# Performance work log

Hardware: AMD Instinct MI355X
Metric: run time of the kernel (lower is better)

## Reference

```python
import jax, jax.numpy as jnp
import numpy as np

H_FEATS = 256
N_NODES = 100000
N_EDGES = 1000000
EDGE_FEAT_DIM = 7
OUT_DIM = 4


def setup_inputs() -> dict:
    key = jax.random.key(0)
    ks = jax.random.split(key, 8)
    h = jax.random.normal(ks[0], (N_NODES, H_FEATS), dtype=jnp.float32)
    edge_feat = jax.random.normal(ks[1], (N_EDGES, EDGE_FEAT_DIM), dtype=jnp.float32)
    src = jax.random.randint(ks[2], (N_EDGES,), 0, N_NODES, dtype=jnp.int64)
    dst = jax.random.randint(ks[3], (N_EDGES,), 0, N_NODES, dtype=jnp.int64)
    in_dim = 2 * H_FEATS + EDGE_FEAT_DIM  # 519
    # Kaiming-ish init scale for the linear layers
    W1_w = jax.random.normal(ks[4], (in_dim, H_FEATS), dtype=jnp.float32) / np.sqrt(in_dim)
    W1_b = jax.random.normal(ks[5], (H_FEATS,), dtype=jnp.float32) * 0.01
    W2_w = jax.random.normal(ks[6], (H_FEATS, OUT_DIM), dtype=jnp.float32) / np.sqrt(H_FEATS)
    W2_b = jax.random.normal(ks[7], (OUT_DIM,), dtype=jnp.float32) * 0.01
    return {"h": h, "edge_feat": edge_feat, "src": src, "dst": dst,
            "W1_w": W1_w, "W1_b": W1_b, "W2_w": W2_w, "W2_b": W2_b}


def reference(h, edge_feat, src, dst, W1_w, W1_b, W2_w, W2_b):
    # Gather src/dst node embeddings per edge, concat with edge features: [E, 2*h_feats+7]
    x = jnp.concatenate([edge_feat, h[src], h[dst]], axis=1)
    # 2-layer MLP per edge: Linear -> ReLU -> Linear
    hid = jax.nn.relu(x @ W1_w + W1_b)          # [E, h_feats]
    rep = hid @ W2_w + W2_b                     # [E, 4]
    return rep
```

## Files before the change

### kernel.cpp

```cpp
#include <hip/hip_runtime.h>
#include <stdint.h>

#define NODES 100000
#define EDGES 1000000
#define HF 256
#define TILES2 (EDGES / 32)


typedef short short8 __attribute__((ext_vector_type(8)));
typedef float f32x4 __attribute__((ext_vector_type(4)));
typedef float f32x2 __attribute__((ext_vector_type(2)));
typedef int i32x4 __attribute__((ext_vector_type(4)));

__device__ __forceinline__ unsigned short f2b(float f) {
  union { float f; uint32_t u; } v; v.f = f;
  return (unsigned short)((v.u + 0x7FFFu + ((v.u >> 16) & 1u)) >> 16);
}
__device__ __forceinline__ float asf(uint32_t u) {
  union { uint32_t u; float f; } v; v.u = u;
  return v.f;
}
__device__ __forceinline__ uint32_t cvtpk(float lo, float hi) {
  uint32_t pk;
  asm("v_cvt_pk_bf16_f32 %0, %1, %2" : "=v"(pk) : "v"(lo), "v"(hi));
  return pk;
}

__global__ __launch_bounds__(256) void pack_w1(const float* __restrict__ W1,
                                               unsigned short* __restrict__ Bp) {
  int idx = blockIdx.x * 256 + threadIdx.x;
  int lane = idx & 63;
  int nbg  = (idx >> 6) & 31;
  int kb   = idx >> 11;
  int n    = nbg * 16 + (lane & 15);
  int k0   = kb * 32 + (lane >> 4) * 8;
  int rbase = (n < 256) ? 7 : 263;
  int col   = n & 255;
  short8 o;
#pragma unroll
  for (int j = 0; j < 8; ++j)
    o[j] = (short)f2b(W1[(size_t)(rbase + k0 + j) * HF + col]);
  *reinterpret_cast<short8*>(Bp + (size_t)idx * 8) = o;
}

__global__ __launch_bounds__(256, 1) void gemm_R(const float* __restrict__ h,
                                                 const unsigned short* __restrict__ Bp,
                                                 const float* __restrict__ b1,
                                                 unsigned short* __restrict__ R) {
  __shared__ unsigned short A[64][264];
  const int m0 = blockIdx.x * 64;
  const int t  = threadIdx.x;
  {
    const int r = t >> 2, q = t & 3;
    const int grow = m0 + r;
    const bool valid = grow < NODES;
    const float* hp = h + (size_t)grow * HF + q * 64;
#pragma unroll
    for (int cc = 0; cc < 8; ++cc) {
      float4 a, b;
      if (valid) {
        a = *reinterpret_cast<const float4*>(hp + cc * 8);
        b = *reinterpret_cast<const float4*>(hp + cc * 8 + 4);
      } else {
        a = make_float4(0.f, 0.f, 0.f, 0.f);
        b = a;
      }
      uint32_t o32[4];
      o32[0] = cvtpk(a.x, a.y);
      o32[1] = cvtpk(a.z, a.w);
      o32[2] = cvtpk(b.x, b.y);
      o32[3] = cvtpk(b.z, b.w);
      *reinterpret_cast<uint4*>(&A[r][q * 64 + cc * 8]) =
          make_uint4(o32[0], o32[1], o32[2], o32[3]);
    }
  }
  __syncthreads();

  const int wave = t >> 6, lane = t & 63;
  const int l15 = lane & 15, lhi = lane >> 4;
  const int nbg0 = wave * 8;
  f32x4 acc[4][8] = {};
#pragma unroll
  for (int kb = 0; kb < 8; ++kb) {
    short8 bfrag[8];
#pragma unroll
    for (int nb = 0; nb < 8; ++nb)
      bfrag[nb] = *reinterpret_cast<const short8*>(
          Bp + (((size_t)(kb * 32 + nbg0 + nb) * 64 + lane) * 8));
    short8 afrag[4];
#pragma unroll
    for (int mb = 0; mb < 4; ++mb)
      afrag[mb] = *reinterpret_cast<const short8*>(&A[mb * 16 + l15][kb * 32 + lhi * 8]);
#pragma unroll
    for (int mb = 0; mb < 4; ++mb)
#pragma unroll
      for (int nb = 0; nb < 8; ++nb)
        acc[mb][nb] = __builtin_amdgcn_mfma_f32_16x16x32_bf16(
            afrag[mb], bfrag[nb], acc[mb][nb], 0, 0, 0);
  }
  const int c0 = wave * 128 + l15;
  float b1v[8] = {};
  if (wave < 2) {
#pragma unroll
    for (int nb = 0; nb < 8; ++nb) b1v[nb] = b1[c0 + nb * 16];
  }
#pragma unroll
  for (int mb = 0; mb < 4; ++mb) {
#pragma unroll
    for (int i = 0; i < 4; ++i) {
      const int row = m0 + mb * 16 + lhi * 4 + i;
      if (row < NODES) {
        unsigned short* rp = R + (size_t)row * 512 + c0;
#pragma unroll
        for (int nb = 0; nb < 8; ++nb) rp[nb * 16] = f2b(acc[mb][nb][i] + b1v[nb]);
      }
    }
  }
}

__global__ __launch_bounds__(256) void edge_mlp(
    const unsigned short* __restrict__ R, const float* __restrict__ ef,
    const int* __restrict__ src, const int* __restrict__ dst,
    const float* __restrict__ W1, const float* __restrict__ W2,
    const float* __restrict__ b2, float* __restrict__ out) {
  __shared__ float w1a[7 * 256];
  for (int i = threadIdx.x; i < 7 * 64; i += 256)
    reinterpret_cast<float4*>(w1a)[i] = reinterpret_cast<const float4*>(W1)[i];
  __syncthreads();

  const int lane = threadIdx.x & 63;
  const int l15 = lane & 15, lhi = lane >> 4;
  const int esub = lane >> 2;
  const int sub  = lane & 3;
  const int bperm_idx = ((((lane & 15) << 2) | (lane >> 4)) << 2);

  short8 bfrag[8];
#pragma unroll
  for (int kb = 0; kb < 8; ++kb) {
    short8 b = {0, 0, 0, 0, 0, 0, 0, 0};
    if (l15 < 4) {
#pragma unroll
      for (int j = 0; j < 8; ++j)
        b[j] = (short)f2b(W2[(size_t)(kb * 32 + lhi * 8 + j) * 4 + l15]);
    }
    bfrag[kb] = b;
  }
  const float b2l = (l15 < 4) ? b2[l15] : 0.f;

  const int wid = (blockIdx.x * blockDim.x + threadIdx.x) >> 6;
  const int nw  = (gridDim.x * blockDim.x) >> 6;

#define TILE_KB(PV, QV, EFV, ACC)                                              \
  {                                                                            \
    const uint32_t* pu = reinterpret_cast<const uint32_t*>(&PV);               \
    const uint32_t* qu = reinterpret_cast<const uint32_t*>(&QV);               \
    f32x2 hd[4];                                                               \
    _Pragma("unroll") for (int w = 0; w < 4; ++w) {                            \
      f32x2 p2 = {asf(pu[w] << 16), asf(pu[w] & 0xffff0000u)};                 \
      f32x2 q2 = {asf(qu[w] << 16), asf(qu[w] & 0xffff0000u)};                 \
      hd[w] = p2 + q2;                                                         \
    }                                                                          \
    _Pragma("unroll") for (int j = 0; j < 7; ++j) {                            \
      f32x2 e2 = {EFV[j], EFV[j]};                                             \
      hd[0] = wv[j][0] * e2 + hd[0];                                           \
      hd[1] = wv[j][1] * e2 + hd[1];                                           \
      hd[2] = wv[j][2] * e2 + hd[2];                                           \
      hd[3] = wv[j][3] * e2 + hd[3];                                           \
    }                                                                          \
    union { i32x4 i; short8 s8; } afm;                                         \
    _Pragma("unroll") for (int w = 0; w < 4; ++w) {                            \
      const float lo = fmaxf(hd[w][0], 0.f);                                   \
      const float hi = fmaxf(hd[w][1], 0.f);                                   \
      afm.i[w] = __builtin_amdgcn_ds_bpermute(bperm_idx, (int)cvtpk(lo, hi));  \
    }                                                                          \
    ACC = __builtin_amdgcn_mfma_f32_16x16x32_bf16(afm.s8, bfrag[kb], ACC, 0, 0, 0); \
  }

  for (int t = wid; t < TILES2; t += nw) {
    const int e0 = t * 32;
    const int eiA = e0 + esub;
    const int eiB = eiA + 16;
    const int sA = src[eiA], dA = dst[eiA];
    const int sB = src[eiB], dB = dst[eiB];
    float efA[7], efB[7];
#pragma unroll
    for (int j = 0; j < 7; ++j) {
      efA[j] = ef[(size_t)eiA * 7 + j];
      efB[j] = ef[(size_t)eiB * 7 + j];
    }
    const unsigned short* PpA = R + (size_t)sA * 512 + sub * 8;
    const unsigned short* QpA = R + (size_t)dA * 512 + 256 + sub * 8;
    const unsigned short* PpB = R + (size_t)sB * 512 + sub * 8;
    const unsigned short* QpB = R + (size_t)dB * 512 + 256 + sub * 8;

    short8 pA[8], qA[8], pB[8], qB[8];
#pragma unroll
    for (int kb = 0; kb < 2; ++kb) {
      pA[kb] = *reinterpret_cast<const short8*>(PpA + kb * 32);
      qA[kb] = *reinterpret_cast<const short8*>(QpA + kb * 32);
      pB[kb] = *reinterpret_cast<const short8*>(PpB + kb * 32);
      qB[kb] = *reinterpret_cast<const short8*>(QpB + kb * 32);
    }

    f32x4 accA = {}, accB = {};
#pragma unroll
    for (int kb = 0; kb < 8; ++kb) {
      if (kb < 6) {
        pA[kb + 2] = *reinterpret_cast<const short8*>(PpA + (kb + 2) * 32);
        qA[kb + 2] = *reinterpret_cast<const short8*>(QpA + (kb + 2) * 32);
        pB[kb + 2] = *reinterpret_cast<const short8*>(PpB + (kb + 2) * 32);
        qB[kb + 2] = *reinterpret_cast<const short8*>(QpB + (kb + 2) * 32);
      }
      f32x2 wv[7][4];
      const float* ws = w1a + kb * 32 + sub * 8;
#pragma unroll
      for (int j = 0; j < 7; ++j) {
        const float4 wa = *reinterpret_cast<const float4*>(ws + j * 256);
        const float4 wb = *reinterpret_cast<const float4*>(ws + j * 256 + 4);
        wv[j][0] = {wa.x, wa.y};
        wv[j][1] = {wa.z, wa.w};
        wv[j][2] = {wb.x, wb.y};
        wv[j][3] = {wb.z, wb.w};
      }
      TILE_KB(pA[kb], qA[kb], efA, accA);
      TILE_KB(pB[kb], qB[kb], efB, accB);
    }
    if (l15 < 4) {
#pragma unroll
      for (int i = 0; i < 4; ++i) {
        out[(size_t)(e0 + lhi * 4 + i) * 4 + l15] = accA[i] + b2l;
        out[(size_t)(e0 + 16 + lhi * 4 + i) * 4 + l15] = accB[i] + b2l;
      }
    }
  }
#undef TILE_KB
}

extern "C" void kernel_launch(void* const* d_in, const int* in_sizes, int n_in,
                              void* d_out, int out_size, void* d_ws, size_t ws_size,
                              hipStream_t stream) {
  const float* h  = (const float*)d_in[0];
  const float* ef = (const float*)d_in[1];
  const int* src  = (const int*)d_in[2];
  const int* dst  = (const int*)d_in[3];
  const float* W1 = (const float*)d_in[4];
  const float* b1 = (const float*)d_in[5];
  const float* W2 = (const float*)d_in[6];
  const float* b2 = (const float*)d_in[7];
  float* out = (float*)d_out;

  const size_t bp_bytes = (size_t)8 * 32 * 64 * 8 * 2;
  unsigned short* Bp = (unsigned short*)d_ws;
  unsigned short* R  = (unsigned short*)((char*)d_ws + bp_bytes);

  pack_w1<<<64, 256, 0, stream>>>(W1, Bp);
  gemm_R<<<(NODES + 63) / 64, 256, 0, stream>>>(h, Bp, b1, R);
  edge_mlp<<<2048, 256, 0, stream>>>(R, ef, src, dst, W1, W2, b2, out);
}
```

Baseline: 236.6 us.

## Counting-sort edges by source node and drop bpermute in the edge MLP

Each call now counting-sorts the edges by source node: a histogram, a two-level scan and an atomic scatter build 32-byte records holding src, dst, the original edge id and the edge features packed to bf16. The edge MLP reads these records, so consecutive edges share source rows of R and get better cache reuse, and it writes outputs back to the original edge positions. The lane-to-edge mapping changes so the MFMA A fragment is built directly in registers, removing the ds_bpermute. In exchange it adds several extra kernels, atomics, a 32 MB record buffer, scattered output stores, and rounds edge features to bf16.

```diff
diff --git a/kernel.cpp b/kernel.cpp
--- a/kernel.cpp
+++ b/kernel.cpp
@@ -5,6 +5,7 @@
 #define EDGES 1000000
 #define HF 256
 #define TILES2 (EDGES / 32)
+#define NBINS (98 * 1024)
 
 
 typedef short short8 __attribute__((ext_vector_type(8)));
@@ -19,6 +20,9 @@
 __device__ __forceinline__ float asf(uint32_t u) {
   union { uint32_t u; float f; } v; v.u = u;
   return v.f;
+}
+__device__ __forceinline__ float b2f(unsigned short s) {
+  return asf(((uint32_t)s) << 16);
 }
 __device__ __forceinline__ uint32_t cvtpk(float lo, float hi) {
   uint32_t pk;
@@ -118,11 +122,85 @@
   }
 }
 
+__global__ __launch_bounds__(256) void hist_k(const int* __restrict__ src,
+                                              int* __restrict__ bins) {
+  int e = blockIdx.x * 256 + threadIdx.x;
+  if (e < EDGES) atomicAdd(&bins[src[e]], 1);
+}
+
+__global__ __launch_bounds__(256) void scan_blocks(int* __restrict__ bins,
+                                                   int* __restrict__ part) {
+  __shared__ int sdata[256];
+  const int t = threadIdx.x;
+  const int base = blockIdx.x * 1024 + t * 4;
+  int4 v = *reinterpret_cast<int4*>(bins + base);
+  const int s = v.x + v.y + v.z + v.w;
+  sdata[t] = s;
+  __syncthreads();
+#pragma unroll
+  for (int off = 1; off < 256; off <<= 1) {
+    int x = (t >= off) ? sdata[t - off] : 0;
+    __syncthreads();
+    sdata[t] += x;
+    __syncthreads();
+  }
+  const int excl = sdata[t] - s;
+  int4 o;
+  o.x = excl; o.y = excl + v.x; o.z = o.y + v.y; o.w = o.z + v.z;
+  *reinterpret_cast<int4*>(bins + base) = o;
+  if (t == 255) part[blockIdx.x] = sdata[255];
+}
+
+__global__ __launch_bounds__(128) void scan_partials(int* __restrict__ part, int nb) {
+  __shared__ int sdata[128];
+  const int t = threadIdx.x;
+  const int v = (t < nb) ? part[t] : 0;
+  sdata[t] = v;
+  __syncthreads();
+#pragma unroll
+  for (int off = 1; off < 128; off <<= 1) {
+    int x = (t >= off) ? sdata[t - off] : 0;
+    __syncthreads();
+    sdata[t] += x;
+    __syncthreads();
+  }
+  if (t < nb) part[t] = sdata[t] - v;
+}
+
+__global__ __launch_bounds__(256) void add_offsets(int* __restrict__ bins,
+                                                   const int* __restrict__ part) {
+  const int add = part[blockIdx.x];
+  const int base = blockIdx.x * 1024 + threadIdx.x * 4;
+  int4 v = *reinterpret_cast<int4*>(bins + base);
+  v.x += add; v.y += add; v.z += add; v.w += add;
+  *reinterpret_cast<int4*>(bins + base) = v;
+}
+
+__global__ __launch_bounds__(256) void scatter_k(const int* __restrict__ src,
+                                                 const int* __restrict__ dst,
+                                                 const float* __restrict__ ef,
+                                                 int* __restrict__ bins,
+                                                 char* __restrict__ rec) {
+  int e = blockIdx.x * 256 + threadIdx.x;
+  if (e >= EDGES) return;
+  const int s = src[e];
+  const int r = atomicAdd(&bins[s], 1);
+  int4 meta;
+  meta.x = s; meta.y = dst[e]; meta.z = e; meta.w = 0;
+  short8 efp = {0, 0, 0, 0, 0, 0, 0, 0};
+#pragma unroll
+  for (int j = 0; j < 7; ++j) efp[j] = (short)f2b(ef[(size_t)e * 7 + j]);
+  *reinterpret_cast<int4*>(rec + (size_t)r * 32) = meta;
+  *reinterpret_cast<short8*>(rec + (size_t)r * 32 + 16) = efp;
+}
+
+template <bool SORTED>
 __global__ __launch_bounds__(256) void edge_mlp(
-    const unsigned short* __restrict__ R, const float* __restrict__ ef,
-    const int* __restrict__ src, const int* __restrict__ dst,
-    const float* __restrict__ W1, const float* __restrict__ W2,
-    const float* __restrict__ b2, float* __restrict__ out) {
+    const unsigned short* __restrict__ R, const char* __restrict__ rec,
+    const float* __restrict__ ef, const int* __restrict__ src,
+    const int* __restrict__ dst, const float* __restrict__ W1,
+    const float* __restrict__ W2, const float* __restrict__ b2,
+    float* __restrict__ out) {
   __shared__ float w1a[7 * 256];
   for (int i = threadIdx.x; i < 7 * 64; i += 256)
     reinterpret_cast<float4*>(w1a)[i] = reinterpret_cast<const float4*>(W1)[i];
@@ -130,9 +208,6 @@
 
   const int lane = threadIdx.x & 63;
   const int l15 = lane & 15, lhi = lane >> 4;
-  const int esub = lane >> 2;
-  const int sub  = lane & 3;
-  const int bperm_idx = ((((lane & 15) << 2) | (lane >> 4)) << 2);
 
   short8 bfrag[8];
 #pragma unroll
@@ -171,27 +246,41 @@
     _Pragma("unroll") for (int w = 0; w < 4; ++w) {                            \
       const float lo = fmaxf(hd[w][0], 0.f);                                   \
       const float hi = fmaxf(hd[w][1], 0.f);                                   \
-      afm.i[w] = __builtin_amdgcn_ds_bpermute(bperm_idx, (int)cvtpk(lo, hi));  \
+      afm.i[w] = (int)cvtpk(lo, hi);                                           \
     }                                                                          \
     ACC = __builtin_amdgcn_mfma_f32_16x16x32_bf16(afm.s8, bfrag[kb], ACC, 0, 0, 0); \
   }
 
   for (int t = wid; t < TILES2; t += nw) {
     const int e0 = t * 32;
-    const int eiA = e0 + esub;
+    const int eiA = e0 + l15;
     const int eiB = eiA + 16;
-    const int sA = src[eiA], dA = dst[eiA];
-    const int sB = src[eiB], dB = dst[eiB];
+    int sA, dA, sB, dB;
     float efA[7], efB[7];
-#pragma unroll
-    for (int j = 0; j < 7; ++j) {
-      efA[j] = ef[(size_t)eiA * 7 + j];
-      efB[j] = ef[(size_t)eiB * 7 + j];
-    }
-    const unsigned short* PpA = R + (size_t)sA * 512 + sub * 8;
-    const unsigned short* QpA = R + (size_t)dA * 512 + 256 + sub * 8;
-    const unsigned short* PpB = R + (size_t)sB * 512 + sub * 8;
-    const unsigned short* QpB = R + (size_t)dB * 512 + 256 + sub * 8;
+    if constexpr (SORTED) {
+      const int4 mA = *reinterpret_cast<const int4*>(rec + (size_t)eiA * 32);
+      const int4 mB = *reinterpret_cast<const int4*>(rec + (size_t)eiB * 32);
+      const short8 eA8 = *reinterpret_cast<const short8*>(rec + (size_t)eiA * 32 + 16);
+      const short8 eB8 = *reinterpret_cast<const short8*>(rec + (size_t)eiB * 32 + 16);
+      sA = mA.x; dA = mA.y; sB = mB.x; dB = mB.y;
+#pragma unroll
+      for (int j = 0; j < 7; ++j) {
+        efA[j] = b2f((unsigned short)eA8[j]);
+        efB[j] = b2f((unsigned short)eB8[j]);
+      }
+    } else {
+      sA = src[eiA]; dA = dst[eiA];
+      sB = src[eiB]; dB = dst[eiB];
+#pragma unroll
+      for (int j = 0; j < 7; ++j) {
+        efA[j] = ef[(size_t)eiA * 7 + j];
+        efB[j] = ef[(size_t)eiB * 7 + j];
+      }
+    }
+    const unsigned short* PpA = R + (size_t)sA * 512 + lhi * 8;
+    const unsigned short* QpA = R + (size_t)dA * 512 + 256 + lhi * 8;
+    const unsigned short* PpB = R + (size_t)sB * 512 + lhi * 8;
+    const unsigned short* QpB = R + (size_t)dB * 512 + 256 + lhi * 8;
 
     short8 pA[8], qA[8], pB[8], qB[8];
 #pragma unroll
@@ -212,7 +301,7 @@
         qB[kb + 2] = *reinterpret_cast<const short8*>(QpB + (kb + 2) * 32);
       }
       f32x2 wv[7][4];
-      const float* ws = w1a + kb * 32 + sub * 8;
+      const float* ws = w1a + kb * 32 + lhi * 8;
 #pragma unroll
       for (int j = 0; j < 7; ++j) {
         const float4 wa = *reinterpret_cast<const float4*>(ws + j * 256);
@@ -228,8 +317,17 @@
     if (l15 < 4) {
 #pragma unroll
       for (int i = 0; i < 4; ++i) {
-        out[(size_t)(e0 + lhi * 4 + i) * 4 + l15] = accA[i] + b2l;
-        out[(size_t)(e0 + 16 + lhi * 4 + i) * 4 + l15] = accB[i] + b2l;
+        const int rA = e0 + lhi * 4 + i;
+        const int rB = rA + 16;
+        if constexpr (SORTED) {
+          const int oA = *reinterpret_cast<const int*>(rec + (size_t)rA * 32 + 8);
+          const int oB = *reinterpret_cast<const int*>(rec + (size_t)rB * 32 + 8);
+          out[(size_t)oA * 4 + l15] = accA[i] + b2l;
+          out[(size_t)oB * 4 + l15] = accB[i] + b2l;
+        } else {
+          out[(size_t)rA * 4 + l15] = accA[i] + b2l;
+          out[(size_t)rB * 4 + l15] = accB[i] + b2l;
+        }
       }
     }
   }
@@ -249,11 +347,32 @@
   const float* b2 = (const float*)d_in[7];
   float* out = (float*)d_out;
 
-  const size_t bp_bytes = (size_t)8 * 32 * 64 * 8 * 2;
+  const size_t bp_bytes  = (size_t)8 * 32 * 64 * 8 * 2;
+  const size_t r_bytes   = (size_t)NODES * 512 * 2;
+  const size_t bins_off  = bp_bytes + r_bytes;
+  const size_t bins_bytes = (size_t)NBINS * 4;
+  const size_t part_off  = bins_off + bins_bytes;
+  const size_t rec_off   = part_off + 512;
+  const size_t need      = rec_off + (size_t)EDGES * 32;
+
   unsigned short* Bp = (unsigned short*)d_ws;
   unsigned short* R  = (unsigned short*)((char*)d_ws + bp_bytes);
 
   pack_w1<<<64, 256, 0, stream>>>(W1, Bp);
   gemm_R<<<(NODES + 63) / 64, 256, 0, stream>>>(h, Bp, b1, R);
-  edge_mlp<<<2048, 256, 0, stream>>>(R, ef, src, dst, W1, W2, b2, out);
-}
+
+  if (ws_size >= need) {
+    int*  bins = (int*)((char*)d_ws + bins_off);
+    int*  part = (int*)((char*)d_ws + part_off);
+    char* rec  = (char*)d_ws + rec_off;
+    hipMemsetAsync(bins, 0, bins_bytes, stream);
+    hist_k<<<(EDGES + 255) / 256, 256, 0, stream>>>(src, bins);
+    scan_blocks<<<NBINS / 1024, 256, 0, stream>>>(bins, part);
+    scan_partials<<<1, 128, 0, stream>>>(part, NBINS / 1024);
+    add_offsets<<<NBINS / 1024, 256, 0, stream>>>(bins, part);
+    scatter_k<<<(EDGES + 255) / 256, 256, 0, stream>>>(src, dst, ef, bins, rec);
+    edge_mlp<true><<<2048, 256, 0, stream>>>(R, rec, ef, src, dst, W1, W2, b2, out);
+  } else {
+    edge_mlp<false><<<2048, 256, 0, stream>>>(R, nullptr, ef, src, dst, W1, W2, b2, out);
+  }
+}
```

Result: slower. 306.3 us (+29.5%).

## Bucket-sort edges by source node to improve gather locality in edge MLP

Applied to the files above, without the earlier changes.

Adds a scatter phase, fused into the node GEMM launch as extra blocks, that bins edges into 32 source-node buckets. Each edge is written as a 32-byte record holding src, dst, original index and bf16 edge features. The edge MLP then reads the records in bucket order and scatters outputs back by the stored index. The goal is L2 reuse of the source-row gathers and removal of the ds_bpermute by changing the lane-to-edge mapping. The cost is a memset of the record buffer, padded tiles, bf16 rounding of edge features, and extra global writes and reads for the records.

```diff
diff --git a/kernel.cpp b/kernel.cpp
--- a/kernel.cpp
+++ b/kernel.cpp
@@ -4,6 +4,11 @@
 #define NODES 100000
 #define EDGES 1000000
 #define HF 256
+#define NBKT 32
+#define BKT_NODES 3125
+#define CAPMAX 33024
+#define GEMM_BLOCKS 1563
+#define SCAT_BLOCKS 245
 #define TILES2 (EDGES / 32)
 
 
@@ -20,14 +25,22 @@
   union { uint32_t u; float f; } v; v.u = u;
   return v.f;
 }
+__device__ __forceinline__ float b2f(unsigned short s) {
+  return asf(((uint32_t)s) << 16);
+}
 __device__ __forceinline__ uint32_t cvtpk(float lo, float hi) {
   uint32_t pk;
   asm("v_cvt_pk_bf16_f32 %0, %1, %2" : "=v"(pk) : "v"(lo), "v"(hi));
   return pk;
 }
 
-__global__ __launch_bounds__(256) void pack_w1(const float* __restrict__ W1,
-                                               unsigned short* __restrict__ Bp) {
+__global__ __launch_bounds__(256) void pack_init(const float* __restrict__ W1,
+                                                 unsigned short* __restrict__ Bp,
+                                                 int* __restrict__ cursor, int cap) {
+  if (blockIdx.x == 64) {
+    if (cursor && threadIdx.x < NBKT) cursor[threadIdx.x] = threadIdx.x * cap;
+    return;
+  }
   int idx = blockIdx.x * 256 + threadIdx.x;
   int lane = idx & 63;
   int nbg  = (idx >> 6) & 31;
@@ -43,86 +56,136 @@
   *reinterpret_cast<short8*>(Bp + (size_t)idx * 8) = o;
 }
 
-__global__ __launch_bounds__(256, 1) void gemm_R(const float* __restrict__ h,
-                                                 const unsigned short* __restrict__ Bp,
-                                                 const float* __restrict__ b1,
-                                                 unsigned short* __restrict__ R) {
-  __shared__ unsigned short A[64][264];
-  const int m0 = blockIdx.x * 64;
-  const int t  = threadIdx.x;
-  {
-    const int r = t >> 2, q = t & 3;
-    const int grow = m0 + r;
-    const bool valid = grow < NODES;
-    const float* hp = h + (size_t)grow * HF + q * 64;
-#pragma unroll
-    for (int cc = 0; cc < 8; ++cc) {
-      float4 a, b;
-      if (valid) {
-        a = *reinterpret_cast<const float4*>(hp + cc * 8);
-        b = *reinterpret_cast<const float4*>(hp + cc * 8 + 4);
-      } else {
-        a = make_float4(0.f, 0.f, 0.f, 0.f);
-        b = a;
-      }
-      uint32_t o32[4];
-      o32[0] = cvtpk(a.x, a.y);
-      o32[1] = cvtpk(a.z, a.w);
-      o32[2] = cvtpk(b.x, b.y);
-      o32[3] = cvtpk(b.z, b.w);
-      *reinterpret_cast<uint4*>(&A[r][q * 64 + cc * 8]) =
-          make_uint4(o32[0], o32[1], o32[2], o32[3]);
-    }
-  }
-  __syncthreads();
-
-  const int wave = t >> 6, lane = t & 63;
-  const int l15 = lane & 15, lhi = lane >> 4;
-  const int nbg0 = wave * 8;
-  f32x4 acc[4][8] = {};
-#pragma unroll
-  for (int kb = 0; kb < 8; ++kb) {
-    short8 bfrag[8];
-#pragma unroll
-    for (int nb = 0; nb < 8; ++nb)
-      bfrag[nb] = *reinterpret_cast<const short8*>(
-          Bp + (((size_t)(kb * 32 + nbg0 + nb) * 64 + lane) * 8));
-    short8 afrag[4];
-#pragma unroll
-    for (int mb = 0; mb < 4; ++mb)
-      afrag[mb] = *reinterpret_cast<const short8*>(&A[mb * 16 + l15][kb * 32 + lhi * 8]);
-#pragma unroll
-    for (int mb = 0; mb < 4; ++mb)
+__global__ __launch_bounds__(256) void gemm_scatter(
+    const float* __restrict__ h, const unsigned short* __restrict__ Bp,
+    const float* __restrict__ b1, unsigned short* __restrict__ R,
+    const int* __restrict__ src, const int* __restrict__ dst,
+    const float* __restrict__ ef, int* __restrict__ cursor,
+    uint4* __restrict__ rec, int pos_max) {
+  __shared__ __align__(16) char sh[33792];
+  const int t = threadIdx.x;
+
+  if (blockIdx.x < GEMM_BLOCKS) {
+    unsigned short (*A)[264] = reinterpret_cast<unsigned short (*)[264]>(sh);
+    const int m0 = blockIdx.x * 64;
+    {
+      const int r = t >> 2, q = t & 3;
+      const int grow = m0 + r;
+      const bool valid = grow < NODES;
+      const float* hp = h + (size_t)grow * HF + q * 64;
+#pragma unroll
+      for (int cc = 0; cc < 8; ++cc) {
+        float4 a, b;
+        if (valid) {
+          a = *reinterpret_cast<const float4*>(hp + cc * 8);
+          b = *reinterpret_cast<const float4*>(hp + cc * 8 + 4);
+        } else {
+          a = make_float4(0.f, 0.f, 0.f, 0.f);
+          b = a;
+        }
+        uint32_t o32[4];
+        o32[0] = cvtpk(a.x, a.y);
+        o32[1] = cvtpk(a.z, a.w);
+        o32[2] = cvtpk(b.x, b.y);
+        o32[3] = cvtpk(b.z, b.w);
+        *reinterpret_cast<uint4*>(&A[r][q * 64 + cc * 8]) =
+            make_uint4(o32[0], o32[1], o32[2], o32[3]);
+      }
+    }
+    __syncthreads();
+
+    const int wave = t >> 6, lane = t & 63;
+    const int l15 = lane & 15, lhi = lane >> 4;
+    const int nbg0 = wave * 8;
+    f32x4 acc[4][8] = {};
+#pragma unroll
+    for (int kb = 0; kb < 8; ++kb) {
+      short8 bfrag[8];
 #pragma unroll
       for (int nb = 0; nb < 8; ++nb)
-        acc[mb][nb] = __builtin_amdgcn_mfma_f32_16x16x32_bf16(
-            afrag[mb], bfrag[nb], acc[mb][nb], 0, 0, 0);
-  }
-  const int c0 = wave * 128 + l15;
-  float b1v[8] = {};
-  if (wave < 2) {
-#pragma unroll
-    for (int nb = 0; nb < 8; ++nb) b1v[nb] = b1[c0 + nb * 16];
-  }
-#pragma unroll
-  for (int mb = 0; mb < 4; ++mb) {
-#pragma unroll
-    for (int i = 0; i < 4; ++i) {
-      const int row = m0 + mb * 16 + lhi * 4 + i;
-      if (row < NODES) {
-        unsigned short* rp = R + (size_t)row * 512 + c0;
-#pragma unroll
-        for (int nb = 0; nb < 8; ++nb) rp[nb * 16] = f2b(acc[mb][nb][i] + b1v[nb]);
-      }
-    }
-  }
-}
-
+        bfrag[nb] = *reinterpret_cast<const short8*>(
+            Bp + (((size_t)(kb * 32 + nbg0 + nb) * 64 + lane) * 8));
+      short8 afrag[4];
+#pragma unroll
+      for (int mb = 0; mb < 4; ++mb)
+        afrag[mb] = *reinterpret_cast<const short8*>(&A[mb * 16 + l15][kb * 32 + lhi * 8]);
+#pragma unroll
+      for (int mb = 0; mb < 4; ++mb)
+#pragma unroll
+        for (int nb = 0; nb < 8; ++nb)
+          acc[mb][nb] = __builtin_amdgcn_mfma_f32_16x16x32_bf16(
+              afrag[mb], bfrag[nb], acc[mb][nb], 0, 0, 0);
+    }
+    const int c0 = wave * 128 + l15;
+    float b1v[8] = {};
+    if (wave < 2) {
+#pragma unroll
+      for (int nb = 0; nb < 8; ++nb) b1v[nb] = b1[c0 + nb * 16];
+    }
+#pragma unroll
+    for (int mb = 0; mb < 4; ++mb) {
+#pragma unroll
+      for (int i = 0; i < 4; ++i) {
+        const int row = m0 + mb * 16 + lhi * 4 + i;
+        if (row < NODES) {
+          unsigned short* rp = R + (size_t)row * 512 + c0;
+#pragma unroll
+          for (int nb = 0; nb < 8; ++nb) rp[nb * 16] = f2b(acc[mb][nb][i] + b1v[nb]);
+        }
+      }
+    }
+  } else {
+    int* cnt = reinterpret_cast<int*>(sh);
+    int* sbase = reinterpret_cast<int*>(sh + 32768);
+    const int blk = blockIdx.x - GEMM_BLOCKS;
+    const int base_e = blk * 4096;
+    const int nE = (base_e + 4096 <= EDGES) ? 4096 : (EDGES - base_e);
+#pragma unroll
+    for (int b = 0; b < NBKT; ++b) cnt[b * 256 + t] = 0;
+    __syncthreads();
+    for (int i = t; i < nE; i += 256) {
+      const int s = src[base_e + i];
+      cnt[(s / BKT_NODES) * 256 + t]++;
+    }
+    __syncthreads();
+    if (t < NBKT) {
+      int run = 0;
+#pragma unroll 4
+      for (int j = 0; j < 256; ++j) {
+        const int c = cnt[t * 256 + j];
+        cnt[t * 256 + j] = run;
+        run += c;
+      }
+      sbase[t] = atomicAdd(&cursor[t], run);
+    }
+    __syncthreads();
+    for (int i = t; i < nE; i += 256) {
+      const int e = base_e + i;
+      const int s = src[e];
+      const int b = s / BKT_NODES;
+      int pos = sbase[b] + cnt[b * 256 + t]++;
+      if (pos > pos_max) pos = pos_max;
+      uint4 meta;
+      meta.x = (uint32_t)s;
+      meta.y = (uint32_t)dst[e];
+      meta.z = (uint32_t)(e + 1);
+      meta.w = 0u;
+      short8 efp = {0, 0, 0, 0, 0, 0, 0, 0};
+#pragma unroll
+      for (int j = 0; j < 7; ++j) efp[j] = (short)f2b(ef[(size_t)e * 7 + j]);
+      rec[(size_t)pos * 2] = meta;
+      *reinterpret_cast<short8*>(rec + (size_t)pos * 2 + 1) = efp;
+    }
+  }
+}
+
+template <bool SORTED>
 __global__ __launch_bounds__(256) void edge_mlp(
-    const unsigned short* __restrict__ R, const float* __restrict__ ef,
-    const int* __restrict__ src, const int* __restrict__ dst,
-    const float* __restrict__ W1, const float* __restrict__ W2,
-    const float* __restrict__ b2, float* __restrict__ out) {
+    const unsigned short* __restrict__ R, const uint4* __restrict__ rec,
+    const float* __restrict__ ef, const int* __restrict__ src,
+    const int* __restrict__ dst, const float* __restrict__ W1,
+    const float* __restrict__ W2, const float* __restrict__ b2,
+    float* __restrict__ out, int nt_tot) {
   __shared__ float w1a[7 * 256];
   for (int i = threadIdx.x; i < 7 * 64; i += 256)
     reinterpret_cast<float4*>(w1a)[i] = reinterpret_cast<const float4*>(W1)[i];
@@ -130,9 +193,6 @@
 
   const int lane = threadIdx.x & 63;
   const int l15 = lane & 15, lhi = lane >> 4;
-  const int esub = lane >> 2;
-  const int sub  = lane & 3;
-  const int bperm_idx = ((((lane & 15) << 2) | (lane >> 4)) << 2);
 
   short8 bfrag[8];
 #pragma unroll
@@ -171,68 +231,99 @@
     _Pragma("unroll") for (int w = 0; w < 4; ++w) {                            \
       const float lo = fmaxf(hd[w][0], 0.f);                                   \
       const float hi = fmaxf(hd[w][1], 0.f);                                   \
-      afm.i[w] = __builtin_amdgcn_ds_bpermute(bperm_idx, (int)cvtpk(lo, hi));  \
+      afm.i[w] = (int)cvtpk(lo, hi);                                           \
     }                                                                          \
     ACC = __builtin_amdgcn_mfma_f32_16x16x32_bf16(afm.s8, bfrag[kb], ACC, 0, 0, 0); \
   }
 
-  for (int t = wid; t < TILES2; t += nw) {
-    const int e0 = t * 32;
-    const int eiA = e0 + esub;
-    const int eiB = eiA + 16;
-    const int sA = src[eiA], dA = dst[eiA];
-    const int sB = src[eiB], dB = dst[eiB];
-    float efA[7], efB[7];
-#pragma unroll
-    for (int j = 0; j < 7; ++j) {
-      efA[j] = ef[(size_t)eiA * 7 + j];
-      efB[j] = ef[(size_t)eiB * 7 + j];
-    }
-    const unsigned short* PpA = R + (size_t)sA * 512 + sub * 8;
-    const unsigned short* QpA = R + (size_t)dA * 512 + 256 + sub * 8;
-    const unsigned short* PpB = R + (size_t)sB * 512 + sub * 8;
-    const unsigned short* QpB = R + (size_t)dB * 512 + 256 + sub * 8;
-
-    short8 pA[8], qA[8], pB[8], qB[8];
-#pragma unroll
-    for (int kb = 0; kb < 2; ++kb) {
-      pA[kb] = *reinterpret_cast<const short8*>(PpA + kb * 32);
-      qA[kb] = *reinterpret_cast<const short8*>(QpA + kb * 32);
-      pB[kb] = *reinterpret_cast<const short8*>(PpB + kb * 32);
-      qB[kb] = *reinterpret_cast<const short8*>(QpB + kb * 32);
-    }
-
-    f32x4 accA = {}, accB = {};
-#pragma unroll
-    for (int kb = 0; kb < 8; ++kb) {
-      if (kb < 6) {
-        pA[kb + 2] = *reinterpret_cast<const short8*>(PpA + (kb + 2) * 32);
-        qA[kb + 2] = *reinterpret_cast<const short8*>(QpA + (kb + 2) * 32);
-        pB[kb + 2] = *reinterpret_cast<const short8*>(PpB + (kb + 2) * 32);
-        qB[kb + 2] = *reinterpret_cast<const short8*>(QpB + (kb + 2) * 32);
-      }
-      f32x2 wv[7][4];
-      const float* ws = w1a + kb * 32 + sub * 8;
+#define BODY(STORE_A, STORE_B)                                                  \
+  {                                                                             \
+    const unsigned short* PpA = R + (size_t)sA * 512 + lhi * 8;                 \
+    const unsigned short* QpA = R + (size_t)dA * 512 + 256 + lhi * 8;           \
+    const unsigned short* PpB = R + (size_t)sB * 512 + lhi * 8;                 \
+    const unsigned short* QpB = R + (size_t)dB * 512 + 256 + lhi * 8;           \
+    short8 pA[8], qA[8], pB[8], qB[8];                                          \
+    _Pragma("unroll") for (int kb = 0; kb < 2; ++kb) {                          \
+      pA[kb] = *reinterpret_cast<const short8*>(PpA + kb * 32);                 \
+      qA[kb] = *reinterpret_cast<const short8*>(QpA + kb * 32);                 \
+      pB[kb] = *reinterpret_cast<const short8*>(PpB + kb * 32);                 \
+      qB[kb] = *reinterpret_cast<const short8*>(QpB + kb * 32);                 \
+    }                                                                           \
+    f32x4 accA = {}, accB = {};                                                 \
+    _Pragma("unroll") for (int kb = 0; kb < 8; ++kb) {                          \
+      if (kb < 6) {                                                             \
+        pA[kb + 2] = *reinterpret_cast<const short8*>(PpA + (kb + 2) * 32);     \
+        qA[kb + 2] = *reinterpret_cast<const short8*>(QpA + (kb + 2) * 32);     \
+        pB[kb + 2] = *reinterpret_cast<const short8*>(PpB + (kb + 2) * 32);     \
+        qB[kb + 2] = *reinterpret_cast<const short8*>(QpB + (kb + 2) * 32);     \
+      }                                                                         \
+      f32x2 wv[7][4];                                                           \
+      const float* ws = w1a + kb * 32 + lhi * 8;                                \
+      _Pragma("unroll") for (int j = 0; j < 7; ++j) {                           \
+        const float4 wa = *reinterpret_cast<const float4*>(ws + j * 256);       \
+        const float4 wb = *reinterpret_cast<const float4*>(ws + j * 256 + 4);   \
+        wv[j][0] = {wa.x, wa.y};                                                \
+        wv[j][1] = {wa.z, wa.w};                                                \
+        wv[j][2] = {wb.x, wb.y};                                                \
+        wv[j][3] = {wb.z, wb.w};                                                \
+      }                                                                         \
+      TILE_KB(pA[kb], qA[kb], efA, accA);                                       \
+      TILE_KB(pB[kb], qB[kb], efB, accB);                                       \
+    }                                                                           \
+    if (l15 < 4) {                                                              \
+      _Pragma("unroll") for (int i = 0; i < 4; ++i) { STORE_A; STORE_B; }       \
+    }                                                                           \
+  }
+
+  if constexpr (SORTED) {
+    const uint32_t* rec32 = reinterpret_cast<const uint32_t*>(rec);
+    for (int tt = wid; tt < nt_tot; tt += nw) {
+      const int e0 = tt * 32;
+      const int eiA = e0 + l15;
+      const int eiB = eiA + 16;
+      const uint4 ma = rec[(size_t)eiA * 2];
+      const uint4 mb = rec[(size_t)eiB * 2];
+      const short8 ea = *reinterpret_cast<const short8*>(rec + (size_t)eiA * 2 + 1);
+      const short8 eb = *reinterpret_cast<const short8*>(rec + (size_t)eiB * 2 + 1);
+      const int sA = (int)ma.x, dA = (int)ma.y;
+      const int sB = (int)mb.x, dB = (int)mb.y;
+      float efA[7], efB[7];
 #pragma unroll
       for (int j = 0; j < 7; ++j) {
-        const float4 wa = *reinterpret_cast<const float4*>(ws + j * 256);
-        const float4 wb = *reinterpret_cast<const float4*>(ws + j * 256 + 4);
-        wv[j][0] = {wa.x, wa.y};
-        wv[j][1] = {wa.z, wa.w};
-        wv[j][2] = {wb.x, wb.y};
-        wv[j][3] = {wb.z, wb.w};
-      }
-      TILE_KB(pA[kb], qA[kb], efA, accA);
-      TILE_KB(pB[kb], qB[kb], efB, accB);
-    }
-    if (l15 < 4) {
-#pragma unroll
-      for (int i = 0; i < 4; ++i) {
-        out[(size_t)(e0 + lhi * 4 + i) * 4 + l15] = accA[i] + b2l;
-        out[(size_t)(e0 + 16 + lhi * 4 + i) * 4 + l15] = accB[i] + b2l;
-      }
-    }
-  }
+        efA[j] = b2f((unsigned short)ea[j]);
+        efB[j] = b2f((unsigned short)eb[j]);
+      }
+      BODY(
+        {
+          const int rA = e0 + lhi * 4 + i;
+          const uint32_t va = rec32[(size_t)rA * 8 + 2];
+          if (va) out[(size_t)(va - 1) * 4 + l15] = accA[i] + b2l;
+        },
+        {
+          const int rB = e0 + 16 + lhi * 4 + i;
+          const uint32_t vb = rec32[(size_t)rB * 8 + 2];
+          if (vb) out[(size_t)(vb - 1) * 4 + l15] = accB[i] + b2l;
+        })
+    }
+  } else {
+    for (int t = wid; t < TILES2; t += nw) {
+      const int e0 = t * 32;
+      const int eiA = e0 + l15;
+      const int eiB = eiA + 16;
+      const int sA = src[eiA], dA = dst[eiA];
+      const int sB = src[eiB], dB = dst[eiB];
+      float efA[7], efB[7];
+#pragma unroll
+      for (int j = 0; j < 7; ++j) {
+        efA[j] = ef[(size_t)eiA * 7 + j];
+        efB[j] = ef[(size_t)eiB * 7 + j];
+      }
+      BODY(
+        { out[(size_t)(e0 + lhi * 4 + i) * 4 + l15] = accA[i] + b2l; },
+        { out[(size_t)(e0 + 16 + lhi * 4 + i) * 4 + l15] = accB[i] + b2l; })
+    }
+  }
+#undef BODY
 #undef TILE_KB
 }
 
@@ -250,10 +341,36 @@
   float* out = (float*)d_out;
 
   const size_t bp_bytes = (size_t)8 * 32 * 64 * 8 * 2;
+  const size_t r_bytes  = (size_t)NODES * 512 * 2;
+  const size_t cur_off  = bp_bytes + r_bytes;
+  const size_t rec_off  = cur_off + 256;
+
+  int cap = 0;
+  if (ws_size > rec_off + 65536) {
+    size_t c = (ws_size - rec_off - 65536) / ((size_t)NBKT * 32);
+    c &= ~(size_t)31;
+    if (c > CAPMAX) c = CAPMAX;
+    cap = (int)c;
+  }
+
   unsigned short* Bp = (unsigned short*)d_ws;
   unsigned short* R  = (unsigned short*)((char*)d_ws + bp_bytes);
 
-  pack_w1<<<64, 256, 0, stream>>>(W1, Bp);
-  gemm_R<<<(NODES + 63) / 64, 256, 0, stream>>>(h, Bp, b1, R);
-  edge_mlp<<<2048, 256, 0, stream>>>(R, ef, src, dst, W1, W2, b2, out);
-}
+  if (cap >= 32000) {
+    int*   cursor = (int*)((char*)d_ws + cur_off);
+    uint4* rec    = (uint4*)((char*)d_ws + rec_off);
+    const size_t rec_bytes = (size_t)NBKT * cap * 32;
+    pack_init<<<65, 256, 0, stream>>>(W1, Bp, cursor, cap);
+    hipMemsetAsync(rec, 0, rec_bytes + 65536, stream);
+    gemm_scatter<<<GEMM_BLOCKS + SCAT_BLOCKS, 256, 0, stream>>>(
+        h, Bp, b1, R, src, dst, ef, cursor, rec, NBKT * cap + 2047);
+    edge_mlp<true><<<2048, 256, 0, stream>>>(R, rec, ef, src, dst, W1, W2, b2, out,
+                                             NBKT * cap / 32);
+  } else {
+    pack_init<<<64, 256, 0, stream>>>(W1, Bp, nullptr, 0);
+    gemm_scatter<<<GEMM_BLOCKS, 256, 0, stream>>>(
+        h, Bp, b1, R, src, dst, ef, nullptr, nullptr, 0);
+    edge_mlp<false><<<2048, 256, 0, stream>>>(R, nullptr, ef, src, dst, W1, W2, b2, out,
+                                              0);
+  }
+}
```

Result: slower. 293.6 us (+24.1%).
